# Optimization experiments

Hardware: AMD Instinct MI355X
Metric: run time of the kernel (lower is better)

## Reference

```python
import jax, jax.numpy as jnp
import numpy as np

B, H, W, C = 4, 256, 256, 192
WS, SHIFT, NH = 8, 4, 6
HD = C // NH            # 32
N = WS * WS             # 64 tokens per window
NW = (H // WS) * (W // WS)  # 1024 windows per image
HIDDEN = 4 * C
SCALE = HD ** -0.5
EPS = 1e-5


def _swin_attn_mask():
    # standard Swin shifted-window mask: 0 where tokens share a region, -100 otherwise
    img = np.zeros((H, W), np.float32)
    cnt = 0
    for hs in (slice(0, -WS), slice(-WS, -SHIFT), slice(-SHIFT, None)):
        for ws_ in (slice(0, -WS), slice(-WS, -SHIFT), slice(-SHIFT, None)):
            img[hs, ws_] = cnt
            cnt += 1
    mw = img.reshape(H // WS, WS, W // WS, WS).transpose(0, 2, 1, 3).reshape(-1, N)
    diff = mw[:, None, :] - mw[:, :, None]
    return np.where(diff != 0, -100.0, 0.0).astype(np.float32)  # (NW, N, N)


def _rel_pos_index():
    coords = np.stack(np.meshgrid(np.arange(WS), np.arange(WS), indexing='ij')).reshape(2, -1)
    rel = (coords[:, :, None] - coords[:, None, :]).transpose(1, 2, 0)
    rel[:, :, 0] += WS - 1
    rel[:, :, 1] += WS - 1
    rel[:, :, 0] *= 2 * WS - 1
    return rel.sum(-1).astype(np.int32)  # (N, N)


def setup_inputs() -> dict:
    key = jax.random.key(0)
    ks = jax.random.split(key, 12)
    s = 0.02
    x = jax.random.normal(ks[0], (B, H * W, C), jnp.float32)
    mask_matrix = jnp.asarray(_swin_attn_mask())
    rel_idx = jnp.asarray(_rel_pos_index())
    return {
        'x': x,
        'mask_matrix': mask_matrix,
        'rel_idx': rel_idx,
        'qkv_w': jax.random.normal(ks[1], (3 * C, C), jnp.float32) * s,
        'qkv_b': jnp.zeros((3 * C,), jnp.float32),
        'proj_w': jax.random.normal(ks[2], (C, C), jnp.float32) * s,
        'proj_b': jnp.zeros((C,), jnp.float32),
        'rpb_table': jax.random.normal(ks[3], ((2 * WS - 1) * (2 * WS - 1), NH), jnp.float32) * s,
        'norm1_g': jnp.ones((C,), jnp.float32),
        'norm1_b': jnp.zeros((C,), jnp.float32),
        'norm2_g': jnp.ones((C,), jnp.float32),
        'norm2_b': jnp.zeros((C,), jnp.float32),
        'fc1_w': jax.random.normal(ks[4], (HIDDEN, C), jnp.float32) * s,
        'fc1_b': jnp.zeros((HIDDEN,), jnp.float32),
        'fc2_w': jax.random.normal(ks[5], (C, HIDDEN), jnp.float32) * s,
        'fc2_b': jnp.zeros((C,), jnp.float32),
    }


def _layernorm(y, g, b):
    mu = y.mean(-1, keepdims=True)
    var = ((y - mu) ** 2).mean(-1, keepdims=True)
    return (y - mu) * jax.lax.rsqrt(var + EPS) * g + b


def reference(x, mask_matrix, rel_idx, qkv_w, qkv_b, proj_w, proj_b, rpb_table,
              norm1_g, norm1_b, norm2_g, norm2_b, fc1_w, fc1_b, fc2_w, fc2_b):
    shortcut = x
    xi = x.reshape(B, H, W, C)
    # cyclic shift (H,W already multiples of WS -> no padding needed)
    xs = jnp.roll(xi, (-SHIFT, -SHIFT), (1, 2))
    # window partition -> (B*NW, N, C)
    win = xs.reshape(B, H // WS, WS, W // WS, WS, C).transpose(0, 1, 3, 2, 4, 5).reshape(-1, N, C)
    B_ = win.shape[0]
    qkv = (win @ qkv_w.T + qkv_b).reshape(B_, N, 3, NH, HD).transpose(2, 0, 3, 1, 4)
    q, k, v = qkv[0] * SCALE, qkv[1], qkv[2]        # (B_, NH, N, HD)
    attn = jnp.einsum('bhnd,bhmd->bhnm', q, k)       # (B_, NH, N, N)
    rpb = rpb_table[rel_idx.reshape(-1)].reshape(N, N, NH).transpose(2, 0, 1)
    attn = attn + rpb[None]
    nWm = mask_matrix.shape[0]
    attn = attn.reshape(B_ // nWm, nWm, NH, N, N) + mask_matrix[None, :, None]
    attn = jax.nn.softmax(attn.reshape(B_, NH, N, N), axis=-1)
    out = jnp.einsum('bhnm,bhmd->bhnd', attn, v).transpose(0, 2, 1, 3).reshape(B_, N, C)
    out = out @ proj_w.T + proj_b
    # window reverse + reverse shift
    xr = out.reshape(B, H // WS, W // WS, WS, WS, C).transpose(0, 1, 3, 2, 4, 5).reshape(B, H, W, C)
    xr = jnp.roll(xr, (SHIFT, SHIFT), (1, 2)).reshape(B, H * W, C)
    x1 = shortcut + _layernorm(xr, norm1_g, norm1_b)  # post-norm residual as in source
    h = jax.nn.gelu(x1 @ fc1_w.T + fc1_b, approximate=False)
    m = h @ fc2_w.T + fc2_b
    return x1 + _layernorm(m, norm2_g, norm2_b)
```

## Files before the change

kernel.cpp:

```cpp
#include <hip/hip_runtime.h>
#include <hip/hip_bf16.h>
#include <math.h>

typedef unsigned short u16;
typedef unsigned int   u32;
typedef __attribute__((ext_vector_type(8))) short bf16x8;
typedef __attribute__((ext_vector_type(4))) float f32x4;

__device__ __forceinline__ u16 f2bf(float f){
  u32 u = __float_as_uint(f);
  u += 0x7fffu + ((u>>16)&1u);
  return (u16)(u>>16);
}
__device__ __forceinline__ u32 pack2(float a, float b){
  return (u32)f2bf(a) | ((u32)f2bf(b)<<16);
}
__device__ __forceinline__ float2 LDF2(const float* p){ return *(const float2*)p; }
__device__ __forceinline__ float gelu_f(float v){
  float t = __expf(1.5957691216057308f * fmaf(0.044715f*v, v*v, v));
  return v - v/(t + 1.0f);
}

#define ST_U32(p,v) (*(u32*)(p) = (v))
#define MFMA16(a,b,c) __builtin_amdgcn_mfma_f32_16x16x32_bf16((a),(b),(c),0,0,0)

__device__ __forceinline__ bf16x8 ldsfrag(const u16* p){ return *(const bf16x8*)p; }
__device__ __forceinline__ bf16x8 gfrag(const u16* p){ return *(const bf16x8*)p; }

constexpr float SCALE_Q = 0.17677669529663687f;
constexpr float LN_EPS  = 1e-5f;

#define NQKV 110592
#define NPRJ 36864
#define NFC  147456
#define QKV_SLAB 50331648ull
#define WS_WEIGHTS_B 884736ull
#define WS_RPBM_B    98304ull
#define WS_SPLIT_HDR (WS_WEIGHTS_B + 2*WS_RPBM_B)
#define WS_SPLIT_NEED (WS_SPLIT_HDR + 3ull*QKV_SLAB*2ull)

__global__ void k_prep(const float* __restrict__ qkv_w, const float* __restrict__ proj_w,
                       const float* __restrict__ fc1_w, const float* __restrict__ fc2_w,
                       const float* __restrict__ rpb, const int* __restrict__ relidx,
                       u16* __restrict__ qkv_bf, u16* __restrict__ proj_bf,
                       u16* __restrict__ fc1_bf, u16* __restrict__ fc2_bf,
                       float* __restrict__ rpbm, float* __restrict__ rpbmT, int mode)
{
  int stride = gridDim.x * blockDim.x;
  int t = blockIdx.x * blockDim.x + threadIdx.x;
  for (int i = t; i < NQKV; i += stride) qkv_bf[i] = f2bf(qkv_w[i]);
  for (int i = t; i < NPRJ; i += stride) proj_bf[i] = f2bf(proj_w[i]);
  for (int i = t; i < NFC;  i += stride) fc1_bf[i]  = f2bf(fc1_w[i]);
  for (int i = t; i < NFC;  i += stride) fc2_bf[i]  = f2bf(fc2_w[i]);
  for (int i = t; i < 6*4096; i += stride){
    int h = i >> 12, ij = i & 4095;
    rpbm[i] = rpb[relidx[ij]*6 + h];
  }
  if (mode){
    for (int i = t; i < 6*4096; i += stride){
      int h = i >> 12, ij = i & 4095;
      int col = ij >> 6, row = ij & 63;
      rpbmT[i] = rpb[relidx[row*64 + col]*6 + h];
    }
  }
}

__global__ __launch_bounds__(256, 4) void k_qkv(
    const float* __restrict__ x, const u16* __restrict__ qkv_bf,
    const float* __restrict__ qkv_b,
    u16* __restrict__ Qg, u16* __restrict__ Kg, u16* __restrict__ VTg)
{
  __shared__ __align__(16) u16 xw[64*200];
  const int tid = threadIdx.x, wave = tid >> 6, lane = tid & 63;
  const int kg = lane >> 4, l15 = lane & 15;
  const int wi = blockIdx.x, b = wi >> 10, wm = wi & 1023;
  const int wh = wm >> 5, ww = wm & 31;
  const size_t imgbase = (size_t)b * (256*256*192);

  for (int s = tid; s < 64*96; s += 256){
    int t = s / 96, c2 = s - t*96;
    int i = t >> 3, j = t & 7;
    int h0 = ((wh<<3) + i + 4) & 255;
    int w0 = ((ww<<3) + j + 4) & 255;
    float2 v = LDF2(x + imgbase + (size_t)(h0*256 + w0)*192 + c2*2);
    ST_U32(xw + t*200 + c2*2, pack2(v.x, v.y));
  }
  __syncthreads();

  const size_t wbase = (size_t)wi * 12288;
  #pragma unroll 1
  for (int batch = 0; batch < 3; ++batch){
    const int col0 = wave*144 + batch*48;
    f32x4 a[4][3];
    #pragma unroll
    for (int j = 0; j < 3; ++j){
      float bv = qkv_b[col0 + j*16 + l15];
      #pragma unroll
      for (int mt = 0; mt < 4; ++mt) a[mt][j] = {bv, bv, bv, bv};
    }
    #pragma unroll 2
    for (int kt = 0; kt < 6; ++kt){
      bf16x8 af[4];
      #pragma unroll
      for (int mt = 0; mt < 4; ++mt)
        af[mt] = ldsfrag(xw + (mt*16 + l15)*200 + kt*32 + kg*8);
      #pragma unroll
      for (int j = 0; j < 3; ++j){
        bf16x8 bfr = gfrag(qkv_bf + (col0 + j*16 + l15)*192 + kt*32 + kg*8);
        #pragma unroll
        for (int mt = 0; mt < 4; ++mt)
          a[mt][j] = MFMA16(af[mt], bfr, a[mt][j]);
      }
    }
    #pragma unroll
    for (int j = 0; j < 3; ++j){
      int colg = col0 + j*16 + l15;
      if (colg < 192){
        #pragma unroll
        for (int mt = 0; mt < 4; ++mt)
          #pragma unroll
          for (int r = 0; r < 4; ++r)
            Qg[wbase + (size_t)(mt*16 + kg*4 + r)*192 + colg] = f2bf(a[mt][j][r]*SCALE_Q);
      } else if (colg < 384){
        #pragma unroll
        for (int mt = 0; mt < 4; ++mt)
          #pragma unroll
          for (int r = 0; r < 4; ++r)
            Kg[wbase + (size_t)(mt*16 + kg*4 + r)*192 + (colg - 192)] = f2bf(a[mt][j][r]);
      } else {
        #pragma unroll
        for (int mt = 0; mt < 4; ++mt){
          ushort4 pk = { f2bf(a[mt][j][0]), f2bf(a[mt][j][1]),
                         f2bf(a[mt][j][2]), f2bf(a[mt][j][3]) };
          *(ushort4*)(VTg + wbase + (size_t)(colg - 384)*64 + mt*16 + kg*4) = pk;
        }
      }
    }
  }
}

__global__ __launch_bounds__(256, 4) void k_attn2(
    const float* __restrict__ x, const float* __restrict__ mask,
    const float* __restrict__ rpbmT,
    const u16* __restrict__ Qg, const u16* __restrict__ Kg,
    const u16* __restrict__ VTg,
    const u16* __restrict__ proj_bf, const float* __restrict__ proj_b,
    const float* __restrict__ n1g, const float* __restrict__ n1b,
    float* __restrict__ x1)
{
  __shared__ __align__(16) u16 prb[64*72];
  __shared__ __align__(16) u16 obuf[64*200];
  __shared__ float lnred[64*8];

  const int tid = threadIdx.x, wave = tid >> 6, lane = tid & 63;
  const int kg = lane >> 4, l15 = lane & 15;
  const int wi = blockIdx.x, b = wi >> 10, wm = wi & 1023;
  const int wh = wm >> 5, ww = wm & 31;
  const size_t imgbase = (size_t)b * (256*256*192);
  const size_t wbase = (size_t)wi * 12288;

  f32x4 pj[4][3];
  #pragma unroll
  for (int mt = 0; mt < 4; ++mt)
    #pragma unroll
    for (int nt = 0; nt < 3; ++nt){
      float bv = proj_b[wave*48 + nt*16 + l15];
      pj[mt][nt] = {bv, bv, bv, bv};
    }

  #pragma unroll 1
  for (int h = 0; h < 6; ++h){
    const f32x4 z = {0.f, 0.f, 0.f, 0.f};
    bf16x8 qf = gfrag(Qg + wbase + (size_t)(wave*16 + l15)*192 + h*32 + kg*8);
    f32x4 at[4];
    #pragma unroll
    for (int nt = 0; nt < 4; ++nt){
      bf16x8 kf = gfrag(Kg + wbase + (size_t)(nt*16 + l15)*192 + h*32 + kg*8);
      at[nt] = MFMA16(qf, kf, z);
    }
    {
      const float* rb = rpbmT + h*4096;
      const float* mb = mask + (size_t)wm*4096;
      #pragma unroll
      for (int nt = 0; nt < 4; ++nt){
        int cidx = (nt*16 + l15)*64 + wave*16 + kg*4;
        float4 r4 = *(const float4*)(rb + cidx);
        float4 m4 = *(const float4*)(mb + cidx);
        at[nt][0] += r4.x + m4.x;
        at[nt][1] += r4.y + m4.y;
        at[nt][2] += r4.z + m4.z;
        at[nt][3] += r4.w + m4.w;
      }
    }
    #pragma unroll
    for (int r = 0; r < 4; ++r){
      float m0 = fmaxf(fmaxf(at[0][r], at[1][r]), fmaxf(at[2][r], at[3][r]));
      #pragma unroll
      for (int mk = 1; mk < 16; mk <<= 1) m0 = fmaxf(m0, __shfl_xor(m0, mk));
      float s = 0.f;
      #pragma unroll
      for (int nt = 0; nt < 4; ++nt){ at[nt][r] = __expf(at[nt][r] - m0); s += at[nt][r]; }
      #pragma unroll
      for (int mk = 1; mk < 16; mk <<= 1) s += __shfl_xor(s, mk);
      float inv = 1.0f / s;
      #pragma unroll
      for (int nt = 0; nt < 4; ++nt) at[nt][r] *= inv;
    }
    #pragma unroll
    for (int nt = 0; nt < 4; ++nt)
      #pragma unroll
      for (int r = 0; r < 4; ++r)
        prb[(wave*16 + kg*4 + r)*72 + nt*16 + l15] = f2bf(at[nt][r]);
    {
      f32x4 ov[2] = {z, z};
      #pragma unroll
      for (int kt = 0; kt < 2; ++kt){
        bf16x8 pf = ldsfrag(prb + (wave*16 + l15)*72 + kt*32 + kg*8);
        #pragma unroll
        for (int d = 0; d < 2; ++d){
          bf16x8 vf = gfrag(VTg + wbase + (size_t)(h*32 + d*16 + l15)*64 + kt*32 + kg*8);
          ov[d] = MFMA16(pf, vf, ov[d]);
        }
      }
      #pragma unroll
      for (int d = 0; d < 2; ++d)
        #pragma unroll
        for (int r = 0; r < 4; ++r)
          obuf[(wave*16 + kg*4 + r)*200 + h*32 + d*16 + l15] = f2bf(ov[d][r]);
    }
  }
  __syncthreads();

  #pragma unroll 2
  for (int kt = 0; kt < 6; ++kt){
    bf16x8 af[4];
    #pragma unroll
    for (int mt = 0; mt < 4; ++mt)
      af[mt] = ldsfrag(obuf + (mt*16 + l15)*200 + kt*32 + kg*8);
    #pragma unroll
    for (int nt = 0; nt < 3; ++nt){
      bf16x8 bfr = gfrag(proj_bf + (wave*48 + nt*16 + l15)*192 + kt*32 + kg*8);
      #pragma unroll
      for (int mt = 0; mt < 4; ++mt)
        pj[mt][nt] = MFMA16(af[mt], bfr, pj[mt][nt]);
    }
  }

  float gv[3], bv2[3];
  #pragma unroll
  for (int nt = 0; nt < 3; ++nt){
    int c = wave*48 + nt*16 + l15;
    gv[nt] = n1g[c]; bv2[nt] = n1b[c];
  }
  #pragma unroll
  for (int mt = 0; mt < 4; ++mt)
    #pragma unroll
    for (int r = 0; r < 4; ++r){
      float s1 = pj[mt][0][r] + pj[mt][1][r] + pj[mt][2][r];
      float s2 = pj[mt][0][r]*pj[mt][0][r] + pj[mt][1][r]*pj[mt][1][r] + pj[mt][2][r]*pj[mt][2][r];
      #pragma unroll
      for (int mk = 1; mk < 16; mk <<= 1){ s1 += __shfl_xor(s1, mk); s2 += __shfl_xor(s2, mk); }
      if (l15 == 0){
        int t = mt*16 + kg*4 + r;
        lnred[t*8 + wave*2]     = s1;
        lnred[t*8 + wave*2 + 1] = s2;
      }
    }
  __syncthreads();
  #pragma unroll
  for (int mt = 0; mt < 4; ++mt)
    #pragma unroll 1
    for (int r = 0; r < 4; ++r){
      int t = mt*16 + kg*4 + r;
      float a1 = lnred[t*8+0] + lnred[t*8+2] + lnred[t*8+4] + lnred[t*8+6];
      float a2 = lnred[t*8+1] + lnred[t*8+3] + lnred[t*8+5] + lnred[t*8+7];
      float mu = a1 * (1.f/192.f);
      float rs = rsqrtf(a2 * (1.f/192.f) - mu*mu + LN_EPS);
      int i = t >> 3, j = t & 7;
      int h0 = ((wh<<3) + i + 4) & 255, w0 = ((ww<<3) + j + 4) & 255;
      size_t base = imgbase + (size_t)(h0*256 + w0)*192;
      #pragma unroll
      for (int nt = 0; nt < 3; ++nt){
        int c = wave*48 + nt*16 + l15;
        x1[base + c] = x[base + c] + (pj[mt][nt][r] - mu)*rs*gv[nt] + bv2[nt];
      }
    }
}

__global__ __launch_bounds__(256, 3) void k_attn(
    const float* __restrict__ x, const float* __restrict__ mask,
    const float* __restrict__ rpbm, const u16* __restrict__ qkv_bf,
    const float* __restrict__ qkv_b, const u16* __restrict__ proj_bf,
    const float* __restrict__ proj_b, const float* __restrict__ n1g,
    const float* __restrict__ n1b, float* __restrict__ x1)
{
  __shared__ __align__(16) u16 xw[64*200];
  __shared__ __align__(16) u16 qkvh[64*72];
  __shared__ __align__(16) u16 vT[32*72];
  __shared__ __align__(16) u16 prb[64*72];
  __shared__ __align__(16) u16 outh[64*40];
  float* lnred = (float*)outh;

  const int tid  = threadIdx.x;
  const int wave = tid >> 6, lane = tid & 63;
  const int kg   = lane >> 4, l15 = lane & 15;
  const int wi = blockIdx.x;
  const int b  = wi >> 10, wm = wi & 1023;
  const int wh = wm >> 5,  ww = wm & 31;
  const size_t imgbase = (size_t)b * (256*256*192);

  for (int s = tid; s < 64*96; s += 256){
    int t = s / 96, c2 = s - t*96;
    int i = t >> 3, j = t & 7;
    int h0 = ((wh<<3) + i + 4) & 255;
    int w0 = ((ww<<3) + j + 4) & 255;
    float2 v = LDF2(x + imgbase + (size_t)(h0*256 + w0)*192 + c2*2);
    ST_U32(xw + t*200 + c2*2, pack2(v.x, v.y));
  }

  f32x4 pj[4][3];
  #pragma unroll
  for (int mt = 0; mt < 4; ++mt)
    #pragma unroll
    for (int nt = 0; nt < 3; ++nt){
      float bv = proj_b[wave*48 + nt*16 + l15];
      pj[mt][nt] = {bv, bv, bv, bv};
    }
  __syncthreads();

  #pragma unroll 1
  for (int h = 0; h < 6; ++h){
    f32x4 qa[6];
    #pragma unroll
    for (int nt = 0; nt < 6; ++nt){
      float bv = qkv_b[(nt>>1)*192 + h*32 + (nt&1)*16 + l15];
      qa[nt] = {bv, bv, bv, bv};
    }
    #pragma unroll 2
    for (int kt = 0; kt < 6; ++kt){
      bf16x8 af = ldsfrag(xw + (wave*16 + l15)*200 + kt*32 + kg*8);
      #pragma unroll
      for (int nt = 0; nt < 6; ++nt){
        bf16x8 bfr = gfrag(qkv_bf + ((nt>>1)*192 + h*32 + (nt&1)*16 + l15)*192 + kt*32 + kg*8);
        qa[nt] = MFMA16(af, bfr, qa[nt]);
      }
    }
    #pragma unroll
    for (int nt = 0; nt < 2; ++nt)
      #pragma unroll
      for (int r = 0; r < 4; ++r)
        qkvh[(wave*16 + kg*4 + r)*72 + nt*16 + l15] = f2bf(qa[nt][r]*SCALE_Q);
    #pragma unroll
    for (int nt = 2; nt < 4; ++nt)
      #pragma unroll
      for (int r = 0; r < 4; ++r)
        qkvh[(wave*16 + kg*4 + r)*72 + 32 + (nt-2)*16 + l15] = f2bf(qa[nt][r]);
    #pragma unroll
    for (int nt = 4; nt < 6; ++nt)
      #pragma unroll
      for (int r = 0; r < 4; ++r)
        vT[((nt-4)*16 + l15)*72 + wave*16 + kg*4 + r] = f2bf(qa[nt][r]);
    __syncthreads();

    f32x4 at[4];
    {
      const f32x4 z = {0.f, 0.f, 0.f, 0.f};
      bf16x8 qf = ldsfrag(qkvh + (wave*16 + l15)*72 + kg*8);
      #pragma unroll
      for (int nt = 0; nt < 4; ++nt){
        bf16x8 kf = ldsfrag(qkvh + (nt*16 + l15)*72 + 32 + kg*8);
        at[nt] = MFMA16(qf, kf, z);
      }
    }
    {
      const float* rb = rpbm + h*4096;
      const float* mb = mask + (size_t)wm*4096;
      #pragma unroll
      for (int nt = 0; nt < 4; ++nt)
        #pragma unroll
        for (int r = 0; r < 4; ++r){
          int idx = (wave*16 + kg*4 + r)*64 + nt*16 + l15;
          at[nt][r] += rb[idx] + mb[idx];
        }
    }
    #pragma unroll
    for (int r = 0; r < 4; ++r){
      float m0 = fmaxf(fmaxf(at[0][r], at[1][r]), fmaxf(at[2][r], at[3][r]));
      #pragma unroll
      for (int mk = 1; mk < 16; mk <<= 1) m0 = fmaxf(m0, __shfl_xor(m0, mk));
      float s = 0.f;
      #pragma unroll
      for (int nt = 0; nt < 4; ++nt){ at[nt][r] = __expf(at[nt][r] - m0); s += at[nt][r]; }
      #pragma unroll
      for (int mk = 1; mk < 16; mk <<= 1) s += __shfl_xor(s, mk);
      float inv = 1.0f / s;
      #pragma unroll
      for (int nt = 0; nt < 4; ++nt) at[nt][r] *= inv;
    }
    #pragma unroll
    for (int nt = 0; nt < 4; ++nt)
      #pragma unroll
      for (int r = 0; r < 4; ++r)
        prb[(wave*16 + kg*4 + r)*72 + nt*16 + l15] = f2bf(at[nt][r]);

    {
      f32x4 ov[2] = {{0,0,0,0},{0,0,0,0}};
      #pragma unroll
      for (int kt = 0; kt < 2; ++kt){
        bf16x8 pf = ldsfrag(prb + (wave*16 + l15)*72 + kt*32 + kg*8);
        #pragma unroll
        for (int nt = 0; nt < 2; ++nt){
          bf16x8 vf = ldsfrag(vT + (nt*16 + l15)*72 + kt*32 + kg*8);
          ov[nt] = MFMA16(pf, vf, ov[nt]);
        }
      }
      #pragma unroll
      for (int nt = 0; nt < 2; ++nt)
        #pragma unroll
        for (int r = 0; r < 4; ++r)
          outh[(wave*16 + kg*4 + r)*40 + nt*16 + l15] = f2bf(ov[nt][r]);
    }
    __syncthreads();

    {
      bf16x8 pw[3];
      #pragma unroll
      for (int nt = 0; nt < 3; ++nt)
        pw[nt] = gfrag(proj_bf + (wave*48 + nt*16 + l15)*192 + h*32 + kg*8);
      #pragma unroll
      for (int mt = 0; mt < 4; ++mt){
        bf16x8 af = ldsfrag(outh + (mt*16 + l15)*40 + kg*8);
        #pragma unroll
        for (int nt = 0; nt < 3; ++nt)
          pj[mt][nt] = MFMA16(af, pw[nt], pj[mt][nt]);
      }
    }
    __syncthreads();
  }

  float gv[3], bv2[3];
  #pragma unroll
  for (int nt = 0; nt < 3; ++nt){
    int c = wave*48 + nt*16 + l15;
    gv[nt] = n1g[c]; bv2[nt] = n1b[c];
  }
  #pragma unroll
  for (int mt = 0; mt < 4; ++mt)
    #pragma unroll
    for (int r = 0; r < 4; ++r){
      float s1 = pj[mt][0][r] + pj[mt][1][r] + pj[mt][2][r];
      float s2 = pj[mt][0][r]*pj[mt][0][r] + pj[mt][1][r]*pj[mt][1][r] + pj[mt][2][r]*pj[mt][2][r];
      #pragma unroll
      for (int mk = 1; mk < 16; mk <<= 1){ s1 += __shfl_xor(s1, mk); s2 += __shfl_xor(s2, mk); }
      if (l15 == 0){
        int t = mt*16 + kg*4 + r;
        lnred[t*8 + wave*2]     = s1;
        lnred[t*8 + wave*2 + 1] = s2;
      }
    }
  __syncthreads();
  #pragma unroll
  for (int mt = 0; mt < 4; ++mt)
    #pragma unroll 1
    for (int r = 0; r < 4; ++r){
      int t = mt*16 + kg*4 + r;
      float a1 = lnred[t*8+0] + lnred[t*8+2] + lnred[t*8+4] + lnred[t*8+6];
      float a2 = lnred[t*8+1] + lnred[t*8+3] + lnred[t*8+5] + lnred[t*8+7];
      float mu = a1 * (1.f/192.f);
      float rs = rsqrtf(a2 * (1.f/192.f) - mu*mu + LN_EPS);
      int i = t >> 3, j = t & 7;
      int h0 = ((wh<<3) + i + 4) & 255, w0 = ((ww<<3) + j + 4) & 255;
      size_t base = imgbase + (size_t)(h0*256 + w0)*192;
      #pragma unroll
      for (int nt = 0; nt < 3; ++nt){
        int c = wave*48 + nt*16 + l15;
        x1[base + c] = x[base + c] + (pj[mt][nt][r] - mu)*rs*gv[nt] + bv2[nt];
      }
    }
}

__global__ __launch_bounds__(256, 3) void k_mlp(
    float* xio, const u16* __restrict__ fc1_bf,
    const float* __restrict__ fc1_b, const u16* __restrict__ fc2_bf,
    const float* __restrict__ fc2_b, const float* __restrict__ n2g,
    const float* __restrict__ n2b)
{
  __shared__ __align__(16) u16 xt[64*200];
  __shared__ __align__(16) u16 hl[64*200];
  __shared__ float lnred[64*8];

  const int tid  = threadIdx.x;
  const int wave = tid >> 6, lane = tid & 63;
  const int kg   = lane >> 4, l15 = lane & 15;
  const size_t t0 = (size_t)blockIdx.x * 64;

  for (int s = tid; s < 64*96; s += 256){
    int t = s / 96, c2 = s - t*96;
    float2 v = LDF2(xio + (t0 + t)*192 + c2*2);
    ST_U32(xt + t*200 + c2*2, pack2(v.x, v.y));
  }
  f32x4 m2[4][3];
  #pragma unroll
  for (int mt = 0; mt < 4; ++mt)
    #pragma unroll
    for (int nt = 0; nt < 3; ++nt){
      float bv = fc2_b[wave*48 + nt*16 + l15];
      m2[mt][nt] = {bv, bv, bv, bv};
    }
  __syncthreads();

  #pragma unroll 1
  for (int c = 0; c < 4; ++c){
    f32x4 a1[4][3];
    #pragma unroll
    for (int mt = 0; mt < 4; ++mt)
      #pragma unroll
      for (int nt = 0; nt < 3; ++nt){
        float bv = fc1_b[c*192 + wave*48 + nt*16 + l15];
        a1[mt][nt] = {bv, bv, bv, bv};
      }
    #pragma unroll 2
    for (int kt = 0; kt < 6; ++kt){
      bf16x8 af[4];
      #pragma unroll
      for (int mt = 0; mt < 4; ++mt)
        af[mt] = ldsfrag(xt + (mt*16 + l15)*200 + kt*32 + kg*8);
      #pragma unroll
      for (int nt = 0; nt < 3; ++nt){
        bf16x8 bfr = gfrag(fc1_bf + (size_t)(c*192 + wave*48 + nt*16 + l15)*192 + kt*32 + kg*8);
        #pragma unroll
        for (int mt = 0; mt < 4; ++mt)
          a1[mt][nt] = MFMA16(af[mt], bfr, a1[mt][nt]);
      }
    }
    #pragma unroll
    for (int mt = 0; mt < 4; ++mt)
      #pragma unroll
      for (int nt = 0; nt < 3; ++nt)
        #pragma unroll
        for (int r = 0; r < 4; ++r)
          hl[(mt*16 + kg*4 + r)*200 + wave*48 + nt*16 + l15] = f2bf(gelu_f(a1[mt][nt][r]));
    __syncthreads();

    #pragma unroll 2
    for (int kt = 0; kt < 6; ++kt){
      bf16x8 af[4];
      #pragma unroll
      for (int mt = 0; mt < 4; ++mt)
        af[mt] = ldsfrag(hl + (mt*16 + l15)*200 + kt*32 + kg*8);
      #pragma unroll
      for (int nt = 0; nt < 3; ++nt){
        bf16x8 bfr = gfrag(fc2_bf + (size_t)(wave*48 + nt*16 + l15)*768 + c*192 + kt*32 + kg*8);
        #pragma unroll
        for (int mt = 0; mt < 4; ++mt)
          m2[mt][nt] = MFMA16(af[mt], bfr, m2[mt][nt]);
      }
    }
    __syncthreads();
  }

  float gv[3], bv2[3];
  #pragma unroll
  for (int nt = 0; nt < 3; ++nt){
    int cc = wave*48 + nt*16 + l15;
    gv[nt] = n2g[cc]; bv2[nt] = n2b[cc];
  }
  #pragma unroll
  for (int mt = 0; mt < 4; ++mt)
    #pragma unroll
    for (int r = 0; r < 4; ++r){
      float s1 = m2[mt][0][r] + m2[mt][1][r] + m2[mt][2][r];
      float s2 = m2[mt][0][r]*m2[mt][0][r] + m2[mt][1][r]*m2[mt][1][r] + m2[mt][2][r]*m2[mt][2][r];
      #pragma unroll
      for (int mk = 1; mk < 16; mk <<= 1){ s1 += __shfl_xor(s1, mk); s2 += __shfl_xor(s2, mk); }
      if (l15 == 0){
        int t = mt*16 + kg*4 + r;
        lnred[t*8 + wave*2]     = s1;
        lnred[t*8 + wave*2 + 1] = s2;
      }
    }
  __syncthreads();
  #pragma unroll
  for (int mt = 0; mt < 4; ++mt)
    #pragma unroll 1
    for (int r = 0; r < 4; ++r){
      int t = mt*16 + kg*4 + r;
      float a1s = lnred[t*8+0] + lnred[t*8+2] + lnred[t*8+4] + lnred[t*8+6];
      float a2s = lnred[t*8+1] + lnred[t*8+3] + lnred[t*8+5] + lnred[t*8+7];
      float mu = a1s * (1.f/192.f);
      float rs = rsqrtf(a2s * (1.f/192.f) - mu*mu + LN_EPS);
      size_t base = (t0 + t)*192;
      #pragma unroll
      for (int nt = 0; nt < 3; ++nt){
        int cc = wave*48 + nt*16 + l15;
        xio[base + cc] = xio[base + cc] + (m2[mt][nt][r] - mu)*rs*gv[nt] + bv2[nt];
      }
    }
}

extern "C" void kernel_launch(void* const* d_in, const int* in_sizes, int n_in,
                              void* d_out, int out_size, void* d_ws, size_t ws_size,
                              hipStream_t stream)
{
  const float* x      = (const float*)d_in[0];
  const float* mask   = (const float*)d_in[1];
  const int*   relidx = (const int*)d_in[2];
  const float* qkv_w  = (const float*)d_in[3];
  const float* qkv_b  = (const float*)d_in[4];
  const float* proj_w = (const float*)d_in[5];
  const float* proj_b = (const float*)d_in[6];
  const float* rpb    = (const float*)d_in[7];
  const float* n1g    = (const float*)d_in[8];
  const float* n1b    = (const float*)d_in[9];
  const float* n2g    = (const float*)d_in[10];
  const float* n2b    = (const float*)d_in[11];
  const float* fc1_w  = (const float*)d_in[12];
  const float* fc1_b  = (const float*)d_in[13];
  const float* fc2_w  = (const float*)d_in[14];
  const float* fc2_b  = (const float*)d_in[15];
  float* xio = (float*)d_out;

  u16* qkv_bf  = (u16*)d_ws;
  u16* proj_bf = qkv_bf + NQKV;
  u16* fc1_bf  = proj_bf + NPRJ;
  u16* fc2_bf  = fc1_bf + NFC;
  float* rpbm  = (float*)(fc2_bf + NFC);
  float* rpbmT = rpbm + 6*4096;
  u16* Qg = (u16*)((char*)d_ws + WS_SPLIT_HDR);
  u16* Kg = Qg + QKV_SLAB;
  u16* VTg = Kg + QKV_SLAB;

  const int split = (ws_size >= WS_SPLIT_NEED) ? 1 : 0;

  k_prep<<<dim3(512), dim3(256), 0, stream>>>(qkv_w, proj_w, fc1_w, fc2_w,
      rpb, relidx, qkv_bf, proj_bf, fc1_bf, fc2_bf, rpbm, rpbmT, split);
  if (split){
    k_qkv<<<dim3(4096), dim3(256), 0, stream>>>(x, qkv_bf, qkv_b, Qg, Kg, VTg);
    k_attn2<<<dim3(4096), dim3(256), 0, stream>>>(x, mask, rpbmT, Qg, Kg, VTg,
        proj_bf, proj_b, n1g, n1b, xio);
  } else {
    k_attn<<<dim3(4096), dim3(256), 0, stream>>>(x, mask, rpbm, qkv_bf, qkv_b,
        proj_bf, proj_b, n1g, n1b, xio);
  }
  k_mlp<<<dim3(4096), dim3(256), 0, stream>>>(xio, fc1_bf, fc1_b, fc2_bf, fc2_b,
      n2g, n2b);
}
```

Baseline: 939.8 us.

## Emit bf16 copy of x1 from attention and add MLP kernel reading it

The attention epilogue now also writes a bf16 copy of x1 to workspace when enough workspace exists. A new MLP kernel reads its A fragments directly from that bf16 buffer in global memory rather than staging fp32 x1 into LDS. This halves LDS use and raises the occupancy target to 4 blocks. Softmax and GELU divisions are also replaced with the fast hardware reciprocal. The trade-off is an extra 50MB global write, plus repeated global fragment reads in place of LDS reuse. The new path depends on the workspace size.

```diff
diff --git a/kernel.cpp b/kernel.cpp
--- a/kernel.cpp
+++ b/kernel.cpp
@@ -18,7 +18,7 @@
 __device__ __forceinline__ float2 LDF2(const float* p){ return *(const float2*)p; }
 __device__ __forceinline__ float gelu_f(float v){
   float t = __expf(1.5957691216057308f * fmaf(0.044715f*v, v*v, v));
-  return v - v/(t + 1.0f);
+  return v - v*__builtin_amdgcn_rcpf(t + 1.0f);
 }
 
 #define ST_U32(p,v) (*(u32*)(p) = (v))
@@ -37,7 +37,8 @@
 #define WS_WEIGHTS_B 884736ull
 #define WS_RPBM_B    98304ull
 #define WS_SPLIT_HDR (WS_WEIGHTS_B + 2*WS_RPBM_B)
-#define WS_SPLIT_NEED (WS_SPLIT_HDR + 3ull*QKV_SLAB*2ull)
+#define WS_SPLIT_NEED  (WS_SPLIT_HDR + 3ull*QKV_SLAB*2ull)
+#define WS_SPLIT2_NEED (WS_SPLIT_HDR + 4ull*QKV_SLAB*2ull)
 
 __global__ void k_prep(const float* __restrict__ qkv_w, const float* __restrict__ proj_w,
                        const float* __restrict__ fc1_w, const float* __restrict__ fc2_w,
@@ -146,7 +147,7 @@
     const u16* __restrict__ VTg,
     const u16* __restrict__ proj_bf, const float* __restrict__ proj_b,
     const float* __restrict__ n1g, const float* __restrict__ n1b,
-    float* __restrict__ x1)
+    float* __restrict__ x1, u16* __restrict__ x1b)
 {
   __shared__ __align__(16) u16 prb[64*72];
   __shared__ __align__(16) u16 obuf[64*200];
@@ -202,7 +203,7 @@
       for (int nt = 0; nt < 4; ++nt){ at[nt][r] = __expf(at[nt][r] - m0); s += at[nt][r]; }
       #pragma unroll
       for (int mk = 1; mk < 16; mk <<= 1) s += __shfl_xor(s, mk);
-      float inv = 1.0f / s;
+      float inv = __builtin_amdgcn_rcpf(s);
       #pragma unroll
       for (int nt = 0; nt < 4; ++nt) at[nt][r] *= inv;
     }
@@ -267,6 +268,7 @@
       }
     }
   __syncthreads();
+  const bool wx = (x1b != nullptr);
   #pragma unroll
   for (int mt = 0; mt < 4; ++mt)
     #pragma unroll 1
@@ -282,7 +284,9 @@
       #pragma unroll
       for (int nt = 0; nt < 3; ++nt){
         int c = wave*48 + nt*16 + l15;
-        x1[base + c] = x[base + c] + (pj[mt][nt][r] - mu)*rs*gv[nt] + bv2[nt];
+        float y = x[base + c] + (pj[mt][nt][r] - mu)*rs*gv[nt] + bv2[nt];
+        x1[base + c] = y;
+        if (wx) x1b[base + c] = f2bf(y);
       }
     }
 }
@@ -393,7 +397,7 @@
       for (int nt = 0; nt < 4; ++nt){ at[nt][r] = __expf(at[nt][r] - m0); s += at[nt][r]; }
       #pragma unroll
       for (int mk = 1; mk < 16; mk <<= 1) s += __shfl_xor(s, mk);
-      float inv = 1.0f / s;
+      float inv = __builtin_amdgcn_rcpf(s);
       #pragma unroll
       for (int nt = 0; nt < 4; ++nt) at[nt][r] *= inv;
     }
@@ -475,6 +479,111 @@
       for (int nt = 0; nt < 3; ++nt){
         int c = wave*48 + nt*16 + l15;
         x1[base + c] = x[base + c] + (pj[mt][nt][r] - mu)*rs*gv[nt] + bv2[nt];
+      }
+    }
+}
+
+__global__ __launch_bounds__(256, 4) void k_mlp2(
+    float* xio, const u16* __restrict__ x1b,
+    const u16* __restrict__ fc1_bf, const float* __restrict__ fc1_b,
+    const u16* __restrict__ fc2_bf, const float* __restrict__ fc2_b,
+    const float* __restrict__ n2g, const float* __restrict__ n2b)
+{
+  __shared__ __align__(16) u16 hl[64*200];
+  float* const lnred = (float*)hl;
+
+  const int tid  = threadIdx.x;
+  const int wave = tid >> 6, lane = tid & 63;
+  const int kg   = lane >> 4, l15 = lane & 15;
+  const size_t t0 = (size_t)blockIdx.x * 64;
+  const u16* xr = x1b + t0*192;
+
+  f32x4 m2[4][3];
+  #pragma unroll
+  for (int mt = 0; mt < 4; ++mt)
+    #pragma unroll
+    for (int nt = 0; nt < 3; ++nt){
+      float bv = fc2_b[wave*48 + nt*16 + l15];
+      m2[mt][nt] = {bv, bv, bv, bv};
+    }
+
+  #pragma unroll 1
+  for (int c = 0; c < 4; ++c){
+    #pragma unroll 1
+    for (int nt = 0; nt < 3; ++nt){
+      f32x4 a1[4];
+      float bv = fc1_b[c*192 + wave*48 + nt*16 + l15];
+      #pragma unroll
+      for (int mt = 0; mt < 4; ++mt) a1[mt] = {bv, bv, bv, bv};
+      #pragma unroll 2
+      for (int kt = 0; kt < 6; ++kt){
+        bf16x8 bfr = gfrag(fc1_bf + (size_t)(c*192 + wave*48 + nt*16 + l15)*192 + kt*32 + kg*8);
+        #pragma unroll
+        for (int mt = 0; mt < 4; ++mt){
+          bf16x8 af = gfrag(xr + (size_t)(mt*16 + l15)*192 + kt*32 + kg*8);
+          a1[mt] = MFMA16(af, bfr, a1[mt]);
+        }
+      }
+      #pragma unroll
+      for (int mt = 0; mt < 4; ++mt)
+        #pragma unroll
+        for (int r = 0; r < 4; ++r)
+          hl[(mt*16 + kg*4 + r)*200 + wave*48 + nt*16 + l15] = f2bf(gelu_f(a1[mt][r]));
+    }
+    __syncthreads();
+
+    #pragma unroll 2
+    for (int kt = 0; kt < 6; ++kt){
+      bf16x8 af[4];
+      #pragma unroll
+      for (int mt = 0; mt < 4; ++mt)
+        af[mt] = ldsfrag(hl + (mt*16 + l15)*200 + kt*32 + kg*8);
+      #pragma unroll
+      for (int nt = 0; nt < 3; ++nt){
+        bf16x8 bfr = gfrag(fc2_bf + (size_t)(wave*48 + nt*16 + l15)*768 + c*192 + kt*32 + kg*8);
+        #pragma unroll
+        for (int mt = 0; mt < 4; ++mt)
+          m2[mt][nt] = MFMA16(af[mt], bfr, m2[mt][nt]);
+      }
+    }
+    __syncthreads();
+  }
+
+  float gv[3], bv2[3];
+  #pragma unroll
+  for (int nt = 0; nt < 3; ++nt){
+    int cc = wave*48 + nt*16 + l15;
+    gv[nt] = n2g[cc]; bv2[nt] = n2b[cc];
+  }
+  #pragma unroll
+  for (int mt = 0; mt < 4; ++mt)
+    #pragma unroll
+    for (int r = 0; r < 4; ++r){
+      float s1 = m2[mt][0][r] + m2[mt][1][r] + m2[mt][2][r];
+      float s2 = m2[mt][0][r]*m2[mt][0][r] + m2[mt][1][r]*m2[mt][1][r] + m2[mt][2][r]*m2[mt][2][r];
+      #pragma unroll
+      for (int mk = 1; mk < 16; mk <<= 1){ s1 += __shfl_xor(s1, mk); s2 += __shfl_xor(s2, mk); }
+      if (l15 == 0){
+        int t = mt*16 + kg*4 + r;
+        lnred[t*8 + wave*2]     = s1;
+        lnred[t*8 + wave*2 + 1] = s2;
+      }
+    }
+  __syncthreads();
+  #pragma unroll
+  for (int mt = 0; mt < 4; ++mt)
+    #pragma unroll 1
+    for (int r = 0; r < 4; ++r){
+      int t = mt*16 + kg*4 + r;
+      float a1s = lnred[t*8+0] + lnred[t*8+2] + lnred[t*8+4] + lnred[t*8+6];
+      float a2s = lnred[t*8+1] + lnred[t*8+3] + lnred[t*8+5] + lnred[t*8+7];
+      float mu = a1s * (1.f/192.f);
+      float rs = rsqrtf(a2s * (1.f/192.f) - mu*mu + LN_EPS);
+      size_t base = (t0 + t)*192;
+      #pragma unroll
+      for (int nt = 0; nt < 3; ++nt){
+        int cc = wave*48 + nt*16 + l15;
+        xio[base + cc] = xio[base + cc] + (m2[mt][nt][r] - mu)*rs*gv[nt] + bv2[nt];
       }
     }
 }
@@ -626,22 +735,28 @@
   u16* fc2_bf  = fc1_bf + NFC;
   float* rpbm  = (float*)(fc2_bf + NFC);
   float* rpbmT = rpbm + 6*4096;
-  u16* Qg = (u16*)((char*)d_ws + WS_SPLIT_HDR);
-  u16* Kg = Qg + QKV_SLAB;
+  u16* Qg  = (u16*)((char*)d_ws + WS_SPLIT_HDR);
+  u16* Kg  = Qg + QKV_SLAB;
   u16* VTg = Kg + QKV_SLAB;
-
-  const int split = (ws_size >= WS_SPLIT_NEED) ? 1 : 0;
+  u16* x1b = VTg + QKV_SLAB;
+
+  const int tier = (ws_size >= WS_SPLIT2_NEED) ? 2 : (ws_size >= WS_SPLIT_NEED) ? 1 : 0;
 
   k_prep<<<dim3(512), dim3(256), 0, stream>>>(qkv_w, proj_w, fc1_w, fc2_w,
-      rpb, relidx, qkv_bf, proj_bf, fc1_bf, fc2_bf, rpbm, rpbmT, split);
-  if (split){
+      rpb, relidx, qkv_bf, proj_bf, fc1_bf, fc2_bf, rpbm, rpbmT, tier ? 1 : 0);
+  if (tier){
     k_qkv<<<dim3(4096), dim3(256), 0, stream>>>(x, qkv_bf, qkv_b, Qg, Kg, VTg);
     k_attn2<<<dim3(4096), dim3(256), 0, stream>>>(x, mask, rpbmT, Qg, Kg, VTg,
-        proj_bf, proj_b, n1g, n1b, xio);
+        proj_bf, proj_b, n1g, n1b, xio, (tier == 2) ? x1b : (u16*)nullptr);
   } else {
     k_attn<<<dim3(4096), dim3(256), 0, stream>>>(x, mask, rpbm, qkv_bf, qkv_b,
         proj_bf, proj_b, n1g, n1b, xio);
   }
-  k_mlp<<<dim3(4096), dim3(256), 0, stream>>>(xio, fc1_bf, fc1_b, fc2_bf, fc2_b,
-      n2g, n2b);
-}
+  if (tier == 2){
+    k_mlp2<<<dim3(4096), dim3(256), 0, stream>>>(xio, x1b, fc1_bf, fc1_b,
+        fc2_bf, fc2_b, n2g, n2b);
+  } else {
+    k_mlp<<<dim3(4096), dim3(256), 0, stream>>>(xio, fc1_bf, fc1_b, fc2_bf, fc2_b,
+        n2g, n2b);
+  }
+}
```

Result: slower. 1.377 ms (+46.6%).

## Split MLP block across 8 waves and use fast reciprocal in softmax/GELU

Applied to the files above, without the earlier changes.

The MLP kernel now runs 512 threads per block. Waves are split into two row groups and four column groups, so each wave handles 32 tokens instead of 64. It preloads six weight fragments per 16-column tile and iterates over them, which should lower register pressure and raise parallelism per 64-token tile. Each weight fragment is now loaded by twice as many waves, and each wave does fewer MFMAs per load. Separately, exact divisions in softmax and GELU are replaced with the hardware approximate reciprocal, giving slightly lower precision.

```diff
diff --git a/kernel.cpp b/kernel.cpp
--- a/kernel.cpp
+++ b/kernel.cpp
@@ -18,7 +18,7 @@
 __device__ __forceinline__ float2 LDF2(const float* p){ return *(const float2*)p; }
 __device__ __forceinline__ float gelu_f(float v){
   float t = __expf(1.5957691216057308f * fmaf(0.044715f*v, v*v, v));
-  return v - v/(t + 1.0f);
+  return v - v*__builtin_amdgcn_rcpf(t + 1.0f);
 }
 
 #define ST_U32(p,v) (*(u32*)(p) = (v))
@@ -37,7 +37,7 @@
 #define WS_WEIGHTS_B 884736ull
 #define WS_RPBM_B    98304ull
 #define WS_SPLIT_HDR (WS_WEIGHTS_B + 2*WS_RPBM_B)
-#define WS_SPLIT_NEED (WS_SPLIT_HDR + 3ull*QKV_SLAB*2ull)
+#define WS_SPLIT_NEED  (WS_SPLIT_HDR + 3ull*QKV_SLAB*2ull)
 
 __global__ void k_prep(const float* __restrict__ qkv_w, const float* __restrict__ proj_w,
                        const float* __restrict__ fc1_w, const float* __restrict__ fc2_w,
@@ -202,7 +202,7 @@
       for (int nt = 0; nt < 4; ++nt){ at[nt][r] = __expf(at[nt][r] - m0); s += at[nt][r]; }
       #pragma unroll
       for (int mk = 1; mk < 16; mk <<= 1) s += __shfl_xor(s, mk);
-      float inv = 1.0f / s;
+      float inv = __builtin_amdgcn_rcpf(s);
       #pragma unroll
       for (int nt = 0; nt < 4; ++nt) at[nt][r] *= inv;
     }
@@ -393,7 +393,7 @@
       for (int nt = 0; nt < 4; ++nt){ at[nt][r] = __expf(at[nt][r] - m0); s += at[nt][r]; }
       #pragma unroll
       for (int mk = 1; mk < 16; mk <<= 1) s += __shfl_xor(s, mk);
-      float inv = 1.0f / s;
+      float inv = __builtin_amdgcn_rcpf(s);
       #pragma unroll
       for (int nt = 0; nt < 4; ++nt) at[nt][r] *= inv;
     }
@@ -479,7 +479,7 @@
     }
 }
 
-__global__ __launch_bounds__(256, 3) void k_mlp(
+__global__ __launch_bounds__(512, 4) void k_mlp(
     float* xio, const u16* __restrict__ fc1_bf,
     const float* __restrict__ fc1_b, const u16* __restrict__ fc2_bf,
     const float* __restrict__ fc2_b, const float* __restrict__ n2g,
@@ -492,68 +492,68 @@
   const int tid  = threadIdx.x;
   const int wave = tid >> 6, lane = tid & 63;
   const int kg   = lane >> 4, l15 = lane & 15;
+  const int wg   = wave >> 2;
+  const int wc   = wave & 3;
   const size_t t0 = (size_t)blockIdx.x * 64;
 
-  for (int s = tid; s < 64*96; s += 256){
+  for (int s = tid; s < 64*96; s += 512){
     int t = s / 96, c2 = s - t*96;
     float2 v = LDF2(xio + (t0 + t)*192 + c2*2);
     ST_U32(xt + t*200 + c2*2, pack2(v.x, v.y));
   }
-  f32x4 m2[4][3];
-  #pragma unroll
-  for (int mt = 0; mt < 4; ++mt)
+  f32x4 m2[2][3];
+  #pragma unroll
+  for (int mt = 0; mt < 2; ++mt)
     #pragma unroll
     for (int nt = 0; nt < 3; ++nt){
-      float bv = fc2_b[wave*48 + nt*16 + l15];
+      float bv = fc2_b[wc*48 + nt*16 + l15];
       m2[mt][nt] = {bv, bv, bv, bv};
     }
   __syncthreads();
 
   #pragma unroll 1
   for (int c = 0; c < 4; ++c){
-    f32x4 a1[4][3];
-    #pragma unroll
-    for (int mt = 0; mt < 4; ++mt)
-      #pragma unroll
-      for (int nt = 0; nt < 3; ++nt){
-        float bv = fc1_b[c*192 + wave*48 + nt*16 + l15];
-        a1[mt][nt] = {bv, bv, bv, bv};
-      }
-    #pragma unroll 2
-    for (int kt = 0; kt < 6; ++kt){
-      bf16x8 af[4];
-      #pragma unroll
-      for (int mt = 0; mt < 4; ++mt)
-        af[mt] = ldsfrag(xt + (mt*16 + l15)*200 + kt*32 + kg*8);
-      #pragma unroll
-      for (int nt = 0; nt < 3; ++nt){
-        bf16x8 bfr = gfrag(fc1_bf + (size_t)(c*192 + wave*48 + nt*16 + l15)*192 + kt*32 + kg*8);
-        #pragma unroll
-        for (int mt = 0; mt < 4; ++mt)
-          a1[mt][nt] = MFMA16(af[mt], bfr, a1[mt][nt]);
-      }
-    }
-    #pragma unroll
-    for (int mt = 0; mt < 4; ++mt)
-      #pragma unroll
-      for (int nt = 0; nt < 3; ++nt)
+    #pragma unroll 1
+    for (int nt = 0; nt < 3; ++nt){
+      bf16x8 w6[6];
+      #pragma unroll
+      for (int kt = 0; kt < 6; ++kt)
+        w6[kt] = gfrag(fc1_bf + (size_t)(c*192 + wc*48 + nt*16 + l15)*192 + kt*32 + kg*8);
+      f32x4 a1[2];
+      {
+        float bv = fc1_b[c*192 + wc*48 + nt*16 + l15];
+        a1[0] = {bv, bv, bv, bv};
+        a1[1] = a1[0];
+      }
+      #pragma unroll
+      for (int kt = 0; kt < 6; ++kt){
+        #pragma unroll
+        for (int mt = 0; mt < 2; ++mt){
+          bf16x8 af = ldsfrag(xt + (wg*32 + mt*16 + l15)*200 + kt*32 + kg*8);
+          a1[mt] = MFMA16(af, w6[kt], a1[mt]);
+        }
+      }
+      #pragma unroll
+      for (int mt = 0; mt < 2; ++mt)
         #pragma unroll
         for (int r = 0; r < 4; ++r)
-          hl[(mt*16 + kg*4 + r)*200 + wave*48 + nt*16 + l15] = f2bf(gelu_f(a1[mt][nt][r]));
+          hl[(wg*32 + mt*16 + kg*4 + r)*200 + wc*48 + nt*16 + l15] = f2bf(gelu_f(a1[mt][r]));
+    }
     __syncthreads();
 
-    #pragma unroll 2
-    for (int kt = 0; kt < 6; ++kt){
-      bf16x8 af[4];
-      #pragma unroll
-      for (int mt = 0; mt < 4; ++mt)
-        af[mt] = ldsfrag(hl + (mt*16 + l15)*200 + kt*32 + kg*8);
-      #pragma unroll
-      for (int nt = 0; nt < 3; ++nt){
-        bf16x8 bfr = gfrag(fc2_bf + (size_t)(wave*48 + nt*16 + l15)*768 + c*192 + kt*32 + kg*8);
-        #pragma unroll
-        for (int mt = 0; mt < 4; ++mt)
-          m2[mt][nt] = MFMA16(af[mt], bfr, m2[mt][nt]);
+    #pragma unroll 1
+    for (int nt = 0; nt < 3; ++nt){
+      bf16x8 w6[6];
+      #pragma unroll
+      for (int kt = 0; kt < 6; ++kt)
+        w6[kt] = gfrag(fc2_bf + (size_t)(wc*48 + nt*16 + l15)*768 + c*192 + kt*32 + kg*8);
+      #pragma unroll
+      for (int kt = 0; kt < 6; ++kt){
+        #pragma unroll
+        for (int mt = 0; mt < 2; ++mt){
+          bf16x8 af = ldsfrag(hl + (wg*32 + mt*16 + l15)*200 + kt*32 + kg*8);
+          m2[mt][nt] = MFMA16(af, w6[kt], m2[mt][nt]);
+        }
       }
     }
     __syncthreads();
@@ -562,11 +562,11 @@
   float gv[3], bv2[3];
   #pragma unroll
   for (int nt = 0; nt < 3; ++nt){
-    int cc = wave*48 + nt*16 + l15;
+    int cc = wc*48 + nt*16 + l15;
     gv[nt] = n2g[cc]; bv2[nt] = n2b[cc];
   }
   #pragma unroll
-  for (int mt = 0; mt < 4; ++mt)
+  for (int mt = 0; mt < 2; ++mt)
     #pragma unroll
     for (int r = 0; r < 4; ++r){
       float s1 = m2[mt][0][r] + m2[mt][1][r] + m2[mt][2][r];
@@ -574,17 +574,17 @@
       #pragma unroll
       for (int mk = 1; mk < 16; mk <<= 1){ s1 += __shfl_xor(s1, mk); s2 += __shfl_xor(s2, mk); }
       if (l15 == 0){
-        int t = mt*16 + kg*4 + r;
-        lnred[t*8 + wave*2]     = s1;
-        lnred[t*8 + wave*2 + 1] = s2;
+        int t = wg*32 + mt*16 + kg*4 + r;
+        lnred[t*8 + wc*2]     = s1;
+        lnred[t*8 + wc*2 + 1] = s2;
       }
     }
   __syncthreads();
   #pragma unroll
-  for (int mt = 0; mt < 4; ++mt)
+  for (int mt = 0; mt < 2; ++mt)
     #pragma unroll 1
     for (int r = 0; r < 4; ++r){
-      int t = mt*16 + kg*4 + r;
+      int t = wg*32 + mt*16 + kg*4 + r;
       float a1s = lnred[t*8+0] + lnred[t*8+2] + lnred[t*8+4] + lnred[t*8+6];
       float a2s = lnred[t*8+1] + lnred[t*8+3] + lnred[t*8+5] + lnred[t*8+7];
       float mu = a1s * (1.f/192.f);
@@ -592,7 +592,7 @@
       size_t base = (t0 + t)*192;
       #pragma unroll
       for (int nt = 0; nt < 3; ++nt){
-        int cc = wave*48 + nt*16 + l15;
+        int cc = wc*48 + nt*16 + l15;
         xio[base + cc] = xio[base + cc] + (m2[mt][nt][r] - mu)*rs*gv[nt] + bv2[nt];
       }
     }
@@ -626,15 +626,15 @@
   u16* fc2_bf  = fc1_bf + NFC;
   float* rpbm  = (float*)(fc2_bf + NFC);
   float* rpbmT = rpbm + 6*4096;
-  u16* Qg = (u16*)((char*)d_ws + WS_SPLIT_HDR);
-  u16* Kg = Qg + QKV_SLAB;
+  u16* Qg  = (u16*)((char*)d_ws + WS_SPLIT_HDR);
+  u16* Kg  = Qg + QKV_SLAB;
   u16* VTg = Kg + QKV_SLAB;
 
-  const int split = (ws_size >= WS_SPLIT_NEED) ? 1 : 0;
+  const int tier = (ws_size >= WS_SPLIT_NEED) ? 1 : 0;
 
   k_prep<<<dim3(512), dim3(256), 0, stream>>>(qkv_w, proj_w, fc1_w, fc2_w,
-      rpb, relidx, qkv_bf, proj_bf, fc1_bf, fc2_bf, rpbm, rpbmT, split);
-  if (split){
+      rpb, relidx, qkv_bf, proj_bf, fc1_bf, fc2_bf, rpbm, rpbmT, tier);
+  if (tier){
     k_qkv<<<dim3(4096), dim3(256), 0, stream>>>(x, qkv_bf, qkv_b, Qg, Kg, VTg);
     k_attn2<<<dim3(4096), dim3(256), 0, stream>>>(x, mask, rpbmT, Qg, Kg, VTg,
         proj_bf, proj_b, n1g, n1b, xio);
@@ -642,6 +642,6 @@
     k_attn<<<dim3(4096), dim3(256), 0, stream>>>(x, mask, rpbm, qkv_bf, qkv_b,
         proj_bf, proj_b, n1g, n1b, xio);
   }
-  k_mlp<<<dim3(4096), dim3(256), 0, stream>>>(xio, fc1_bf, fc1_b, fc2_bf, fc2_b,
+  k_mlp<<<dim3(4096), dim3(512), 0, stream>>>(xio, fc1_bf, fc1_b, fc2_bf, fc2_b,
       n2g, n2b);
 }
```

New measurement: 1.137 ms. +21.0%, slower.
